# Performance work log

Measured on AMD Instinct MI355X. Metric: run time of the kernel, lower is better.

## Reference

```python
import jax, jax.numpy as jnp
from jax import lax
import numpy as np

SCORE_THRESH = 0.05
NMS_THRESH = 0.5
MAX_DET = 100
MIN_SIZE = 0.01
BBOX_CLIP = float(np.log(1000.0 / 16.0))
NEG = -1e10


def setup_inputs() -> dict:
    key = jax.random.key(0)
    ks = jax.random.split(key, 12)
    N, IN, REP, C = 2000, 256 * 7 * 7, 1024, 91
    box_features = jax.random.normal(ks[0], (N, IN), jnp.float32)
    x1 = jax.random.uniform(ks[1], (N,), jnp.float32, 0.0, 1000.0)
    y1 = jax.random.uniform(ks[2], (N,), jnp.float32, 0.0, 600.0)
    bw = jax.random.uniform(ks[3], (N,), jnp.float32, 16.0, 200.0)
    bh = jax.random.uniform(ks[4], (N,), jnp.float32, 16.0, 180.0)
    proposals = jnp.stack([x1, y1, x1 + bw, y1 + bh], axis=1)
    W1 = jax.random.normal(ks[5], (IN, REP), jnp.float32) * 0.01
    b1 = jnp.zeros((REP,), jnp.float32)
    W2 = jax.random.normal(ks[6], (REP, REP), jnp.float32) * 0.03
    b2 = jnp.zeros((REP,), jnp.float32)
    Wc = jax.random.normal(ks[7], (REP, C), jnp.float32) * 0.1
    bc = jax.random.normal(ks[8], (C,), jnp.float32) * 0.5
    Wr = jax.random.normal(ks[9], (REP, 4 * C), jnp.float32) * 0.01
    br = jnp.zeros((4 * C,), jnp.float32)
    return dict(box_features=box_features, proposals=proposals,
                W1=W1, b1=b1, W2=W2, b2=b2, Wc=Wc, bc=bc, Wr=Wr, br=br,
                image_h=800, image_w=1216)


def _nms(boxes, scores):
    """Greedy NMS with fixed trip count; scores already masked to NEG for invalid."""
    M = boxes.shape[0]
    areas = (boxes[:, 2] - boxes[:, 0]) * (boxes[:, 3] - boxes[:, 1])
    idxs = jnp.arange(M)

    def step(sm, _):
        i = jnp.argmax(sm)
        valid = sm[i] > NEG * 0.5
        b = boxes[i]
        xx1 = jnp.maximum(b[0], boxes[:, 0]); yy1 = jnp.maximum(b[1], boxes[:, 1])
        xx2 = jnp.minimum(b[2], boxes[:, 2]); yy2 = jnp.minimum(b[3], boxes[:, 3])
        inter = jnp.clip(xx2 - xx1, 0.0) * jnp.clip(yy2 - yy1, 0.0)
        iou = inter / (areas[i] + areas - inter + 1e-9)
        suppress = (iou > NMS_THRESH) | (idxs == i)
        sm = jnp.where(valid, jnp.where(suppress, NEG, sm), sm)
        return sm, jnp.where(valid, i, -1)

    _, keep = lax.scan(step, scores, None, length=MAX_DET)
    return keep  # [MAX_DET] int, -1 for padding


def reference(box_features, proposals, W1, b1, W2, b2, Wc, bc, Wr, br, image_h, image_w):
    N = box_features.shape[0]
    C = Wc.shape[1]
    # box head MLP (Linear+ReLU x2) and predictors
    h = jax.nn.relu(box_features @ W1 + b1)
    h = jax.nn.relu(h @ W2 + b2)
    class_logits = h @ Wc + bc                      # [N, C]
    box_reg = (h @ Wr + br).reshape(N, C, 4)        # [N, C, 4]
    # box decode (weights 10,10,5,5) against proposals
    pw = proposals[:, 2] - proposals[:, 0]
    ph = proposals[:, 3] - proposals[:, 1]
    pcx = proposals[:, 0] + 0.5 * pw
    pcy = proposals[:, 1] + 0.5 * ph
    dx = box_reg[..., 0] / 10.0
    dy = box_reg[..., 1] / 10.0
    dw = jnp.minimum(box_reg[..., 2] / 5.0, BBOX_CLIP)
    dh = jnp.minimum(box_reg[..., 3] / 5.0, BBOX_CLIP)
    cx = dx * pw[:, None] + pcx[:, None]
    cy = dy * ph[:, None] + pcy[:, None]
    w = jnp.exp(dw) * pw[:, None]
    hh = jnp.exp(dh) * ph[:, None]
    boxes = jnp.stack([cx - 0.5 * w, cy - 0.5 * hh, cx + 0.5 * w, cy + 0.5 * hh], axis=-1)
    scores = jax.nn.softmax(class_logits, axis=-1)
    # clip to image
    Wim = jnp.float32(image_w); Him = jnp.float32(image_h)
    boxes = jnp.stack([jnp.clip(boxes[..., 0], 0.0, Wim),
                       jnp.clip(boxes[..., 1], 0.0, Him),
                       jnp.clip(boxes[..., 2], 0.0, Wim),
                       jnp.clip(boxes[..., 3], 0.0, Him)], axis=-1)
    # drop background class, flatten to [N*(C-1)]
    boxes = boxes[:, 1:].reshape(-1, 4)
    scores = scores[:, 1:].reshape(-1)
    labels = jnp.broadcast_to(jnp.arange(1, C, dtype=jnp.int32), (N, C - 1)).reshape(-1)
    # score threshold + remove small boxes (as masking, static shapes)
    bw = boxes[:, 2] - boxes[:, 0]
    bh = boxes[:, 3] - boxes[:, 1]
    valid = (scores > SCORE_THRESH) & (bw >= MIN_SIZE) & (bh >= MIN_SIZE)
    sm = jnp.where(valid, scores, NEG)
    # class-aware (batched) NMS via per-class coordinate offsets
    off = labels.astype(boxes.dtype) * (jnp.maximum(Wim, Him) + 1.0)
    keep = _nms(boxes + off[:, None], sm)
    mask = keep >= 0
    idx = jnp.maximum(keep, 0)
    out_boxes = jnp.take(boxes, idx, axis=0) * mask[:, None]
    out_scores = jnp.take(scores, idx) * mask
    out_labels = jnp.take(labels, idx) * mask.astype(jnp.int32)
    return out_boxes, out_scores, out_labels
```

## Files before the change

### kernel.cpp

```cpp
#include <hip/hip_runtime.h>

#define CPC 2000
#define SPC 100
#define NCLS 90
#define TM 128
#define TN 128
#define TKK 16

typedef __attribute__((ext_vector_type(8))) short bf16x8;
typedef __attribute__((ext_vector_type(4))) float f32x4;
typedef __attribute__((ext_vector_type(4))) unsigned short u16x4;

__device__ __forceinline__ unsigned short f2bf_rne(float f) {
    unsigned u = __float_as_uint(f);
    return (unsigned short)((u + 0x7FFFu + ((u >> 16) & 1u)) >> 16);
}
__device__ __forceinline__ unsigned short f2bf_trunc(float f) {
    return (unsigned short)(__float_as_uint(f) >> 16);
}
__device__ __forceinline__ float bfhi_f32(float f) {
    return __uint_as_float(__float_as_uint(f) & 0xFFFF0000u);
}
__device__ __forceinline__ void async_load16(const void* g, void* l) {
    __builtin_amdgcn_global_load_lds((const __attribute__((address_space(1))) unsigned int*)g,
                                     (__attribute__((address_space(3))) unsigned int*)l, 16, 0, 0);
}
__device__ __forceinline__ int swz(int c) { return c ^ ((c >> 3) & 3); }

__device__ __forceinline__ void xcd_remap(unsigned& bx, unsigned& by, unsigned& bz)
{
    const unsigned nx = gridDim.x, ny = gridDim.y;
    const unsigned nwg = nx * ny * gridDim.z;
    unsigned lin = blockIdx.x + nx * (blockIdx.y + ny * blockIdx.z);
    if ((nwg & 7u) == 0u)
        lin = (lin & 7u) * (nwg >> 3) + (lin >> 3);
    bx = lin % nx;
    unsigned rem = lin / nx;
    by = rem % ny;
    bz = rem / ny;
}

__global__ __launch_bounds__(256) void split_transpose(
    const float* __restrict__ W, unsigned short* __restrict__ Thi,
    unsigned short* __restrict__ Tlo, int K, int N)
{
    __shared__ float tile[64][33];
    const int kt = blockIdx.x * 64, nt = blockIdx.y * 32;
    const int tx = threadIdx.x & 31, ty = threadIdx.x >> 5;
#pragma unroll
    for (int j = 0; j < 8; ++j) {
        int k = kt + ty + j * 8, n = nt + tx;
        tile[ty + j * 8][tx] = (k < K && n < N) ? W[(size_t)k * N + n] : 0.f;
    }
    __syncthreads();
#pragma unroll
    for (int j = 0; j < 4; ++j) {
        int n = nt + ty + j * 8;
        int k = kt + tx * 2;
        if (n < N && k < K) {
            float f0 = tile[tx * 2][ty + j * 8];
            float f1 = tile[tx * 2 + 1][ty + j * 8];
            unsigned hi = (unsigned)f2bf_trunc(f0) | ((unsigned)f2bf_trunc(f1) << 16);
            unsigned lo = (unsigned)f2bf_rne(f0 - bfhi_f32(f0))
                        | ((unsigned)f2bf_rne(f1 - bfhi_f32(f1)) << 16);
            *reinterpret_cast<unsigned*>(&Thi[(size_t)n * K + k]) = hi;
            *reinterpret_cast<unsigned*>(&Tlo[(size_t)n * K + k]) = lo;
        }
    }
}

__global__ __launch_bounds__(256) void split_transpose2(
    const float* __restrict__ Wa, const float* __restrict__ Wb, int Na, int Nb,
    unsigned short* __restrict__ Thi, unsigned short* __restrict__ Tlo, int K)
{
    const int N = Na + Nb;
    __shared__ float tile[64][33];
    const int kt = blockIdx.x * 64, nt = blockIdx.y * 32;
    const int tx = threadIdx.x & 31, ty = threadIdx.x >> 5;
#pragma unroll
    for (int j = 0; j < 8; ++j) {
        int k = kt + ty + j * 8, n = nt + tx;
        float v = 0.f;
        if (k < K && n < N)
            v = (n < Na) ? Wa[(size_t)k * Na + n] : Wb[(size_t)k * Nb + (n - Na)];
        tile[ty + j * 8][tx] = v;
    }
    __syncthreads();
#pragma unroll
    for (int j = 0; j < 4; ++j) {
        int n = nt + ty + j * 8;
        int k = kt + tx * 2;
        if (n < N && k < K) {
            float f0 = tile[tx * 2][ty + j * 8];
            float f1 = tile[tx * 2 + 1][ty + j * 8];
            unsigned hi = (unsigned)f2bf_trunc(f0) | ((unsigned)f2bf_trunc(f1) << 16);
            unsigned lo = (unsigned)f2bf_rne(f0 - bfhi_f32(f0))
                        | ((unsigned)f2bf_rne(f1 - bfhi_f32(f1)) << 16);
            *reinterpret_cast<unsigned*>(&Thi[(size_t)n * K + k]) = hi;
            *reinterpret_cast<unsigned*>(&Tlo[(size_t)n * K + k]) = lo;
        }
    }
}

__global__ __launch_bounds__(256, 4) void gemm_bf16x3_f32a(
    const float* __restrict__ A, const unsigned short* __restrict__ Bhi,
    const unsigned short* __restrict__ Blo, float* __restrict__ C,
    int M, int N, int K, int klen)
{
    __shared__ unsigned short Ah[2048], Al[2048], Bh[4096], Bl[4096];
    unsigned bxu, byu, bzu;
    xcd_remap(bxu, byu, bzu);
    const int tid = threadIdx.x;
    const int wv = tid >> 6, ln = tid & 63;
    const int q = ln >> 4, lm = ln & 15;
    const int m0 = byu * 64, n0 = bxu * 128;
    const int k0 = bzu * klen;
    int k1 = k0 + klen; if (k1 > K) k1 = K;
    const int bcol_t = wv * 32;

    f32x4 acc[4][2];
#pragma unroll
    for (int i = 0; i < 4; ++i)
#pragma unroll
        for (int j = 0; j < 2; ++j) acc[i][j] = (f32x4)0.f;

    int gr = m0 + (tid >> 2); if (gr >= M) gr = M - 1;
    const float* Arow = A + (size_t)gr * K + (tid & 3) * 8;
    const int apc = swz(tid);

    unsigned bsrc[2];
#pragma unroll
    for (int i = 0; i < 2; ++i) {
        int s = i * 256 + tid;
        int gn = n0 + (s >> 2); if (gn >= N) gn = N - 1;
        int qe = (s & 3) ^ ((s >> 3) & 3);
        bsrc[i] = (unsigned)gn * (unsigned)K + (unsigned)(qe * 8);
    }

    for (int kt = k0; kt < k1; kt += 32) {
#pragma unroll
        for (int i = 0; i < 2; ++i) {
            async_load16(Bhi + bsrc[i] + kt, &Bh[(i * 256 + wv * 64) * 8]);
            async_load16(Blo + bsrc[i] + kt, &Bl[(i * 256 + wv * 64) * 8]);
        }
        float4 v0 = *reinterpret_cast<const float4*>(Arow + kt);
        float4 v1 = *reinterpret_cast<const float4*>(Arow + kt + 4);
        float f[8] = {v0.x, v0.y, v0.z, v0.w, v1.x, v1.y, v1.z, v1.w};
        bf16x8 hi, lo;
#pragma unroll
        for (int e = 0; e < 8; ++e) {
            hi[e] = (short)f2bf_trunc(f[e]);
            lo[e] = (short)f2bf_rne(f[e] - bfhi_f32(f[e]));
        }
        *(bf16x8*)&Ah[apc * 8] = hi;
        *(bf16x8*)&Al[apc * 8] = lo;
        __syncthreads();

        bf16x8 afh[4], afl[4], bfh[2], bfl[2];
#pragma unroll
        for (int mi = 0; mi < 4; ++mi) {
            int p = swz((mi * 16 + lm) * 4 + q);
            afh[mi] = *(const bf16x8*)&Ah[p * 8];
            afl[mi] = *(const bf16x8*)&Al[p * 8];
        }
#pragma unroll
        for (int ni = 0; ni < 2; ++ni) {
            int p = swz((bcol_t + ni * 16 + lm) * 4 + q);
            bfh[ni] = *(const bf16x8*)&Bh[p * 8];
            bfl[ni] = *(const bf16x8*)&Bl[p * 8];
        }
#pragma unroll
        for (int mi = 0; mi < 4; ++mi)
#pragma unroll
            for (int ni = 0; ni < 2; ++ni) {
                acc[mi][ni] = __builtin_amdgcn_mfma_f32_16x16x32_bf16(afh[mi], bfh[ni], acc[mi][ni], 0, 0, 0);
                acc[mi][ni] = __builtin_amdgcn_mfma_f32_16x16x32_bf16(afl[mi], bfh[ni], acc[mi][ni], 0, 0, 0);
                acc[mi][ni] = __builtin_amdgcn_mfma_f32_16x16x32_bf16(afh[mi], bfl[ni], acc[mi][ni], 0, 0, 0);
            }
        __syncthreads();
    }

    float* Cz = C + (size_t)bzu * (size_t)M * (size_t)N;
#pragma unroll
    for (int mi = 0; mi < 4; ++mi)
#pragma unroll
        for (int ni = 0; ni < 2; ++ni)
#pragma unroll
            for (int ri = 0; ri < 4; ++ri) {
                int rr = m0 + mi * 16 + q * 4 + ri;
                int cc = n0 + bcol_t + ni * 16 + lm;
                if (rr < M && cc < N) Cz[(size_t)rr * N + cc] = acc[mi][ni][ri];
            }
}

__global__ __launch_bounds__(256, 4) void gemm_bf16x3_sa(
    const unsigned short* __restrict__ Ahi_g, const unsigned short* __restrict__ Alo_g,
    const unsigned short* __restrict__ Bhi, const unsigned short* __restrict__ Blo,
    float* __restrict__ C, int M, int N, int K, int klen)
{
    __shared__ unsigned short Ah[2048], Al[2048], Bh[4096], Bl[4096];
    unsigned bxu, byu, bzu;
    xcd_remap(bxu, byu, bzu);
    const int tid = threadIdx.x;
    const int wv = tid >> 6, ln = tid & 63;
    const int q = ln >> 4, lm = ln & 15;
    const int m0 = byu * 64, n0 = bxu * 128;
    const int k0 = bzu * klen;
    int k1 = k0 + klen; if (k1 > K) k1 = K;
    const int bcol_t = wv * 32;

    f32x4 acc[4][2];
#pragma unroll
    for (int i = 0; i < 4; ++i)
#pragma unroll
        for (int j = 0; j < 2; ++j) acc[i][j] = (f32x4)0.f;

    int agr = m0 + (tid >> 2); if (agr >= M) agr = M - 1;
    const unsigned asrc = (unsigned)agr * (unsigned)K
                        + (unsigned)(((tid & 3) ^ ((tid >> 3) & 3)) * 8);

    unsigned bsrc[2];
#pragma unroll
    for (int i = 0; i < 2; ++i) {
        int s = i * 256 + tid;
        int gn = n0 + (s >> 2); if (gn >= N) gn = N - 1;
        int qe = (s & 3) ^ ((s >> 3) & 3);
        bsrc[i] = (unsigned)gn * (unsigned)K + (unsigned)(qe * 8);
    }

    for (int kt = k0; kt < k1; kt += 32) {
        async_load16(Ahi_g + asrc + kt, &Ah[(wv * 64) * 8]);
        async_load16(Alo_g + asrc + kt, &Al[(wv * 64) * 8]);
#pragma unroll
        for (int i = 0; i < 2; ++i) {
            async_load16(Bhi + bsrc[i] + kt, &Bh[(i * 256 + wv * 64) * 8]);
            async_load16(Blo + bsrc[i] + kt, &Bl[(i * 256 + wv * 64) * 8]);
        }
        __syncthreads();

        bf16x8 afh[4], afl[4], bfh[2], bfl[2];
#pragma unroll
        for (int mi = 0; mi < 4; ++mi) {
            int p = swz((mi * 16 + lm) * 4 + q);
            afh[mi] = *(const bf16x8*)&Ah[p * 8];
            afl[mi] = *(const bf16x8*)&Al[p * 8];
        }
#pragma unroll
        for (int ni = 0; ni < 2; ++ni) {
            int p = swz((bcol_t + ni * 16 + lm) * 4 + q);
            bfh[ni] = *(const bf16x8*)&Bh[p * 8];
            bfl[ni] = *(const bf16x8*)&Bl[p * 8];
        }
#pragma unroll
        for (int mi = 0; mi < 4; ++mi)
#pragma unroll
            for (int ni = 0; ni < 2; ++ni) {
                acc[mi][ni] = __builtin_amdgcn_mfma_f32_16x16x32_bf16(afh[mi], bfh[ni], acc[mi][ni], 0, 0, 0);
                acc[mi][ni] = __builtin_amdgcn_mfma_f32_16x16x32_bf16(afl[mi], bfh[ni], acc[mi][ni], 0, 0, 0);
                acc[mi][ni] = __builtin_amdgcn_mfma_f32_16x16x32_bf16(afh[mi], bfl[ni], acc[mi][ni], 0, 0, 0);
            }
        __syncthreads();
    }

    float* Cz = C + (size_t)bzu * (size_t)M * (size_t)N;
#pragma unroll
    for (int mi = 0; mi < 4; ++mi)
#pragma unroll
        for (int ni = 0; ni < 2; ++ni)
#pragma unroll
            for (int ri = 0; ri < 4; ++ri) {
                int rr = m0 + mi * 16 + q * 4 + ri;
                int cc = n0 + bcol_t + ni * 16 + lm;
                if (rr < M && cc < N) Cz[(size_t)rr * N + cc] = acc[mi][ni][ri];
            }
}

__global__ __launch_bounds__(256) void gemm_f32(
    const float* __restrict__ A, const float* __restrict__ B,
    const float* __restrict__ bias, float* __restrict__ C,
    int M, int N, int K, int ksplit, int relu)
{
    __shared__ float As[TKK][TM + 4];
    __shared__ float Bs[TKK][TN + 4];
    const int tid = threadIdx.x;
    const int tx = tid & 15, ty = tid >> 4;
    const int m0 = blockIdx.y * TM, n0 = blockIdx.x * TN;
    const int z = blockIdx.z;
    const int kstart = z * ksplit;
    const int kend = (kstart + ksplit < K) ? (kstart + ksplit) : K;
    float* Cz = C + (size_t)z * (size_t)M * (size_t)N;
    const bool nvec = ((N & 3) == 0);

    float acc[8][8];
#pragma unroll
    for (int i = 0; i < 8; ++i)
#pragma unroll
        for (int j = 0; j < 8; ++j) acc[i][j] = 0.f;

    for (int kt = kstart; kt < kend; kt += TKK) {
#pragma unroll
        for (int l = 0; l < 2; ++l) {
            int idx = tid + l * 256;
            int rr = idx >> 2, kq = idx & 3;
            float4 v = make_float4(0.f, 0.f, 0.f, 0.f);
            int grr = m0 + rr;
            if (grr < M)
                v = *reinterpret_cast<const float4*>(A + (size_t)grr * K + kt + (kq << 2));
            As[(kq << 2) + 0][rr] = v.x;
            As[(kq << 2) + 1][rr] = v.y;
            As[(kq << 2) + 2][rr] = v.z;
            As[(kq << 2) + 3][rr] = v.w;
        }
#pragma unroll
        for (int l = 0; l < 2; ++l) {
            int idx = tid + l * 256;
            int kk = idx >> 5, nq = idx & 31;
            int gn = n0 + (nq << 2);
            const float* bp = B + (size_t)(kt + kk) * N + gn;
            float4 v;
            if (nvec && gn + 3 < N) {
                v = *reinterpret_cast<const float4*>(bp);
            } else {
                v.x = (gn + 0 < N) ? bp[0] : 0.f;
                v.y = (gn + 1 < N) ? bp[1] : 0.f;
                v.z = (gn + 2 < N) ? bp[2] : 0.f;
                v.w = (gn + 3 < N) ? bp[3] : 0.f;
            }
            *reinterpret_cast<float4*>(&Bs[kk][nq << 2]) = v;
        }
        __syncthreads();
#pragma unroll
        for (int kk = 0; kk < TKK; ++kk) {
            float a[8], b[8];
            *reinterpret_cast<float4*>(&a[0]) = *reinterpret_cast<const float4*>(&As[kk][ty * 8]);
            *reinterpret_cast<float4*>(&a[4]) = *reinterpret_cast<const float4*>(&As[kk][ty * 8 + 4]);
            *reinterpret_cast<float4*>(&b[0]) = *reinterpret_cast<const float4*>(&Bs[kk][tx * 4]);
            *reinterpret_cast<float4*>(&b[4]) = *reinterpret_cast<const float4*>(&Bs[kk][64 + tx * 4]);
#pragma unroll
            for (int i = 0; i < 8; ++i)
#pragma unroll
                for (int j = 0; j < 8; ++j)
                    acc[i][j] = fmaf(a[i], b[j], acc[i][j]);
        }
        __syncthreads();
    }
#pragma unroll
    for (int i = 0; i < 8; ++i) {
        int grr = m0 + ty * 8 + i;
        if (grr >= M) continue;
#pragma unroll
        for (int j = 0; j < 8; ++j) {
            int gc = n0 + ((j < 4) ? (tx * 4 + j) : (64 + tx * 4 + (j - 4)));
            if (gc >= N) continue;
            float v = acc[i][j];
            if (bias) v += bias[gc];
            if (relu) v = fmaxf(v, 0.f);
            Cz[(size_t)grr * N + gc] = v;
        }
    }
}

__global__ void combine_bias_act(const float* __restrict__ P, const float* __restrict__ bias,
                                 float* __restrict__ H, int total, int N, int nsplit,
                                 int pstride, int relu)
{
    int i = blockIdx.x * blockDim.x + threadIdx.x;
    if (i >= total) return;
    float s = P[i];
    for (int j = 1; j < nsplit; ++j) s += P[i + (size_t)j * (size_t)pstride];
    s += bias[i % N];
    if (relu) s = fmaxf(s, 0.f);
    H[i] = s;
}

__global__ void combine_bias_split(const float* __restrict__ P, const float* __restrict__ bias,
                                   unsigned short* __restrict__ Hhi, unsigned short* __restrict__ Hlo,
                                   int total, int N, int nsplit, int pstride, int relu)
{
    int i = (blockIdx.x * blockDim.x + threadIdx.x) * 4;
    if (i >= total) return;
    float4 s = *reinterpret_cast<const float4*>(P + i);
    for (int j = 1; j < nsplit; ++j) {
        float4 p = *reinterpret_cast<const float4*>(P + i + (size_t)j * (size_t)pstride);
        s.x += p.x; s.y += p.y; s.z += p.z; s.w += p.w;
    }
    const float4 b = *reinterpret_cast<const float4*>(bias + (i % N));
    s.x += b.x; s.y += b.y; s.z += b.z; s.w += b.w;
    if (relu) {
        s.x = fmaxf(s.x, 0.f); s.y = fmaxf(s.y, 0.f);
        s.z = fmaxf(s.z, 0.f); s.w = fmaxf(s.w, 0.f);
    }
    u16x4 hi = { f2bf_trunc(s.x), f2bf_trunc(s.y), f2bf_trunc(s.z), f2bf_trunc(s.w) };
    u16x4 lo = { f2bf_rne(s.x - bfhi_f32(s.x)), f2bf_rne(s.y - bfhi_f32(s.y)),
                 f2bf_rne(s.z - bfhi_f32(s.z)), f2bf_rne(s.w - bfhi_f32(s.w)) };
    *reinterpret_cast<u16x4*>(&Hhi[i]) = hi;
    *reinterpret_cast<u16x4*>(&Hlo[i]) = lo;
}

__global__ void combine_head(const float* __restrict__ P, const float* __restrict__ bc,
                             const float* __restrict__ br, float* __restrict__ H,
                             int total, int nsplit, int pstride)
{
    int i = (blockIdx.x * blockDim.x + threadIdx.x) * 4;
    if (i >= total) return;
    float4 s = *reinterpret_cast<const float4*>(P + i);
    for (int j = 1; j < nsplit; ++j) {
        float4 p = *reinterpret_cast<const float4*>(P + i + (size_t)j * (size_t)pstride);
        s.x += p.x; s.y += p.y; s.z += p.z; s.w += p.w;
    }
    float sv[4] = {s.x, s.y, s.z, s.w};
#pragma unroll
    for (int e = 0; e < 4; ++e) {
        int col = (i + e) % 455;
        sv[e] += (col < 91) ? bc[col] : br[col - 91];
    }
    *reinterpret_cast<float4*>(&H[i]) = make_float4(sv[0], sv[1], sv[2], sv[3]);
}

__device__ __forceinline__ float scalar_dim(const int* p)
{
    int iv = *p;
    return (iv > 0 && iv < (1 << 20)) ? (float)iv : *reinterpret_cast<const float*>(p);
}

__global__ __launch_bounds__(128) void decode_compact(
    const float* __restrict__ logits, int lstr, const float* __restrict__ breg, int bstr,
    const float4* __restrict__ proposals, const int* __restrict__ ihp,
    const int* __restrict__ iwp,
    float4* __restrict__ cbox, float* __restrict__ cscore, int* __restrict__ cn,
    int* __restrict__ ccnt)
{
    const int n = blockIdx.x;
    const int c = threadIdx.x;
    __shared__ float sl[91];
    __shared__ float red[128];
    if (c < 91) sl[c] = logits[(size_t)n * lstr + c];
    __syncthreads();
    red[c] = (c < 91) ? sl[c] : -3.0e38f;
    __syncthreads();
#pragma unroll
    for (int s = 64; s > 0; s >>= 1) {
        if (c < s) red[c] = fmaxf(red[c], red[c + s]);
        __syncthreads();
    }
    const float s_max = red[0];
    __syncthreads();
    red[c] = (c < 91) ? expf(sl[c] - s_max) : 0.f;
    __syncthreads();
#pragma unroll
    for (int s = 64; s > 0; s >>= 1) {
        if (c < s) red[c] += red[c + s];
        __syncthreads();
    }
    const float s_sum = red[0];
    if (c < 1 || c >= 91) return;

    const float score = expf(sl[c] - s_max) / s_sum;
    const float Wim = scalar_dim(iwp), Him = scalar_dim(ihp);
    float4 p = proposals[n];
    float pw = p.z - p.x, ph = p.w - p.y;
    float pcx = p.x + 0.5f * pw, pcy = p.y + 0.5f * ph;
    const float* r4 = breg + (size_t)n * bstr + c * 4;
    float dxv = r4[0] / 10.f, dyv = r4[1] / 10.f;
    const float BCLIP = 4.135166556742356f;
    float dwv = fminf(r4[2] / 5.f, BCLIP);
    float dhv = fminf(r4[3] / 5.f, BCLIP);
    float cx = dxv * pw + pcx, cy = dyv * ph + pcy;
    float w = expf(dwv) * pw, hh = expf(dhv) * ph;
    float x1 = cx - 0.5f * w, y1 = cy - 0.5f * hh;
    float x2 = cx + 0.5f * w, y2 = cy + 0.5f * hh;
    x1 = fminf(fmaxf(x1, 0.f), Wim);
    y1 = fminf(fmaxf(y1, 0.f), Him);
    x2 = fminf(fmaxf(x2, 0.f), Wim);
    y2 = fminf(fmaxf(y2, 0.f), Him);
    float bw = x2 - x1, bh = y2 - y1;
    if (score > 0.05f && bw >= 0.01f && bh >= 0.01f) {
        int cls = c - 1;
        int pos = atomicAdd(&ccnt[cls], 1);
        if (pos < CPC) {
            cbox[cls * CPC + pos] = make_float4(x1, y1, x2, y2);
            cscore[cls * CPC + pos] = score;
            cn[cls * CPC + pos] = n;
        }
    }
}

__global__ __launch_bounds__(256) void nms_class(
    const float4* __restrict__ cbox, const float* __restrict__ cscore,
    const int* __restrict__ cn, const int* __restrict__ ccnt,
    float4* __restrict__ sbox, float* __restrict__ sscore,
    unsigned long long* __restrict__ skey, int* __restrict__ scnt)
{
    const int cls = blockIdx.x;
    const int tid = threadIdx.x;
    int cnt = ccnt[cls]; if (cnt > CPC) cnt = CPC;

    __shared__ float4 cb[CPC];
    __shared__ unsigned long long keys[CPC];
    __shared__ unsigned long long red[4];
    __shared__ float4 selsh;
    __shared__ int selidx_sh;

    for (int i = tid; i < cnt; i += 256) {
        cb[i] = cbox[cls * CPC + i];
        unsigned int sb = __float_as_uint(cscore[cls * CPC + i]);
        sb ^= (sb >> 31) ? 0xFFFFFFFFu : 0x80000000u;
        unsigned int flat = (unsigned)cn[cls * CPC + i] * 90u + (unsigned)cls;
        keys[i] = ((unsigned long long)sb << 32) | (unsigned long long)(0xFFFFFFFFu - flat);
    }
    __syncthreads();

    int sel = 0;
    while (sel < SPC) {
        unsigned long long best = 0ull;
        for (int i = tid; i < cnt; i += 256) {
            unsigned long long k = keys[i];
            if (k > best) best = k;
        }
#pragma unroll
        for (int d = 32; d >= 1; d >>= 1) {
            unsigned long long o = __shfl_down(best, d, 64);
            if (o > best) best = o;
        }
        if ((tid & 63) == 0) red[tid >> 6] = best;
        __syncthreads();
        unsigned long long gbest = red[0];
        if (red[1] > gbest) gbest = red[1];
        if (red[2] > gbest) gbest = red[2];
        if (red[3] > gbest) gbest = red[3];
        if (gbest == 0ull) break;
        for (int i = tid; i < cnt; i += 256)
            if (keys[i] == gbest) { selsh = cb[i]; selidx_sh = i; }
        __syncthreads();
        float4 s = selsh;
        const int si = selidx_sh;
        const float sa = (s.z - s.x) * (s.w - s.y);
        if (tid == 0) {
            sbox[cls * SPC + sel] = s;
            unsigned int sb = (unsigned int)(gbest >> 32);
            sb ^= (sb >> 31) ? 0x80000000u : 0xFFFFFFFFu;
            sscore[cls * SPC + sel] = __uint_as_float(sb);
            skey[cls * SPC + sel] = gbest;
        }
        for (int i = tid; i < cnt; i += 256) {
            float4 b = cb[i];
            float xx1 = fmaxf(s.x, b.x), yy1 = fmaxf(s.y, b.y);
            float xx2 = fminf(s.z, b.z), yy2 = fminf(s.w, b.w);
            float inter = fmaxf(xx2 - xx1, 0.f) * fmaxf(yy2 - yy1, 0.f);
            float area = (b.z - b.x) * (b.w - b.y);
            if (3.f * inter > sa + area + 1e-9f || i == si) keys[i] = 0ull;
        }
        ++sel;
        __syncthreads();
    }
    if (tid == 0) scnt[cls] = sel;
}

__global__ __launch_bounds__(128) void nms_merge(
    const float4* __restrict__ sbox, const float* __restrict__ sscore,
    const unsigned long long* __restrict__ skey, const int* __restrict__ scnt,
    float* __restrict__ out)
{
    const int tid = threadIdx.x;
    __shared__ int head[NCLS];
    __shared__ unsigned long long red[2];
    __shared__ int selc_sh;
    if (tid < NCLS) head[tid] = 0;
    __syncthreads();

    for (int k = 0; k < 100; ++k) {
        unsigned long long key = 0ull;
        if (tid < NCLS && head[tid] < scnt[tid]) key = skey[tid * SPC + head[tid]];
        unsigned long long mykey = key;
#pragma unroll
        for (int d = 32; d >= 1; d >>= 1) {
            unsigned long long o = __shfl_down(key, d, 64);
            if (o > key) key = o;
        }
        if ((tid & 63) == 0) red[tid >> 6] = key;
        if (tid == 0) selc_sh = -1;
        __syncthreads();
        unsigned long long gbest = red[0] > red[1] ? red[0] : red[1];
        if (gbest != 0ull && mykey == gbest) selc_sh = tid;
        __syncthreads();
        const int c = selc_sh;
        if (tid == 0) {
            if (c >= 0) {
                int h = head[c];
                float4 b = sbox[c * SPC + h];
                out[k * 4 + 0] = b.x; out[k * 4 + 1] = b.y;
                out[k * 4 + 2] = b.z; out[k * 4 + 3] = b.w;
                out[400 + k] = sscore[c * SPC + h];
                out[500 + k] = (float)(c + 1);
            } else {
                out[k * 4 + 0] = 0.f; out[k * 4 + 1] = 0.f;
                out[k * 4 + 2] = 0.f; out[k * 4 + 3] = 0.f;
                out[400 + k] = 0.f; out[500 + k] = 0.f;
            }
        }
        if (c >= 0 && tid == c) head[c]++;
        __syncthreads();
    }
}

extern "C" void kernel_launch(void* const* d_in, const int* in_sizes, int n_in,
                              void* d_out, int out_size, void* d_ws, size_t ws_size,
                              hipStream_t stream)
{
    const float* bf    = (const float*)d_in[0];
    const float* props = (const float*)d_in[1];
    const float* W1    = (const float*)d_in[2];
    const float* b1    = (const float*)d_in[3];
    const float* W2    = (const float*)d_in[4];
    const float* b2    = (const float*)d_in[5];
    const float* Wc    = (const float*)d_in[6];
    const float* bc    = (const float*)d_in[7];
    const float* Wr    = (const float*)d_in[8];
    const float* br    = (const float*)d_in[9];
    const int*   ihp   = (const int*)d_in[10];
    const int*   iwp   = (const int*)d_in[11];
    float* ws  = (float*)d_ws;
    float* out = (float*)d_out;

    const size_t MN   = 2000ull * 1024ull;
    const size_t NLOG = 2000ull * 91ull;
    const size_t NREG = 2000ull * 364ull;
    const size_t NHEAD = 2000ull * 455ull;
    const size_t ws_floats = ws_size / 4;

    const size_t BT1F = 1024ull * 12544ull / 2;
    const size_t WT2F = 1024ull * 1024ull / 2;
    const size_t WHF  = 455ull * 1024ull / 2;
    const size_t NMSF = (size_t)NCLS * CPC * 6 + (size_t)NCLS * SPC * 7 + 256;
    const size_t PF   = 4 * MN;
    const size_t NEED = 2 * BT1F + 2 * WT2F + 2 * WHF + 2 * MN + NHEAD + NMSF + PF + 64;

    if (ws_floats >= NEED) {
        unsigned short* BT1hi = (unsigned short*)ws;
        unsigned short* BT1lo = (unsigned short*)(ws + BT1F);
        unsigned short* WT2hi = (unsigned short*)(ws + 2 * BT1F);
        unsigned short* WT2lo = (unsigned short*)(ws + 2 * BT1F + WT2F);
        unsigned short* WHhi  = (unsigned short*)(ws + 2 * BT1F + 2 * WT2F);
        unsigned short* WHlo  = (unsigned short*)(ws + 2 * BT1F + 2 * WT2F + WHF);
        float* H1   = ws + 2 * BT1F + 2 * WT2F + 2 * WHF;
        float* H2   = H1 + MN;
        float* HEAD = H2 + MN;
        float* CBOX   = HEAD + NHEAD;
        float* CSCORE = CBOX + (size_t)NCLS * CPC * 4;
        int*   CN     = (int*)(CSCORE + (size_t)NCLS * CPC);
        float* SBOX   = (float*)(CN + (size_t)NCLS * CPC);
        float* SSCORE = SBOX + (size_t)NCLS * SPC * 4;
        unsigned long long* SKEY = (unsigned long long*)(SSCORE + (size_t)NCLS * SPC);
        int*   CCNT = (int*)(SKEY + (size_t)NCLS * SPC);
        int*   SCNT = CCNT + NCLS;
        float* P = (float*)(SCNT + NCLS + 64);

        unsigned short* H1hi = (unsigned short*)H1;
        unsigned short* H1lo = H1hi + MN;
        unsigned short* H2hi = (unsigned short*)H2;
        unsigned short* H2lo = H2hi + MN;

        split_transpose<<<dim3(196, 32), 256, 0, stream>>>(W1, BT1hi, BT1lo, 12544, 1024);
        split_transpose<<<dim3(16, 32), 256, 0, stream>>>(W2, WT2hi, WT2lo, 1024, 1024);
        split_transpose2<<<dim3(16, 15), 256, 0, stream>>>(Wc, Wr, 91, 364, WHhi, WHlo, 1024);
        gemm_bf16x3_f32a<<<dim3(8, 32, 4), 256, 0, stream>>>(bf, BT1hi, BT1lo, P,
                                                             2000, 1024, 12544, 3136);
        combine_bias_split<<<(int)(MN / 4 / 256), 256, 0, stream>>>(P, b1, H1hi, H1lo,
                                                             (int)MN, 1024, 4, (int)MN, 1);
        gemm_bf16x3_sa<<<dim3(8, 32, 4), 256, 0, stream>>>(H1hi, H1lo, WT2hi, WT2lo, P,
                                                           2000, 1024, 1024, 256);
        combine_bias_split<<<(int)(MN / 4 / 256), 256, 0, stream>>>(P, b2, H2hi, H2lo,
                                                             (int)MN, 1024, 4, (int)MN, 1);
        gemm_bf16x3_sa<<<dim3(4, 32, 8), 256, 0, stream>>>(H2hi, H2lo, WHhi, WHlo, P,
                                                           2000, 455, 1024, 128);
        combine_head<<<(int)((NHEAD / 4 + 255) / 256), 256, 0, stream>>>(P, bc, br, HEAD,
                                                             (int)NHEAD, 8, (int)NHEAD);
        hipMemsetAsync(CCNT, 0, 2 * NCLS * sizeof(int), stream);
        decode_compact<<<2000, 128, 0, stream>>>(HEAD, 455, HEAD + 91, 455,
                                                 (const float4*)props, ihp, iwp,
                                                 (float4*)CBOX, CSCORE, CN, CCNT);
        nms_class<<<NCLS, 256, 0, stream>>>((const float4*)CBOX, CSCORE, CN, CCNT,
                                            (float4*)SBOX, SSCORE, SKEY, SCNT);
        nms_merge<<<1, 128, 0, stream>>>((const float4*)SBOX, SSCORE, SKEY, SCNT, out);
        return;
    }

    const size_t NMSF2 = (size_t)NCLS * CPC * 6 + (size_t)NCLS * SPC * 7 + 256;
    const size_t TAILF = 2 * MN + NLOG + NREG + NMSF2;
    int z1 = 2;
    if (ws_floats >= TAILF + 8 * MN) z1 = 8;
    else if (ws_floats >= TAILF + 4 * MN) z1 = 4;
    const size_t REUSE = (size_t)z1 * MN;
    int zh = (REUSE >= 8 * NREG) ? 8 : 4;

    float* P      = ws;
    float* H1     = P + REUSE;
    float* H2     = H1 + MN;
    float* LOG    = H2 + MN;
    float* BREG   = LOG + NLOG;
    float* CBOX   = BREG + NREG;
    float* CSCORE = CBOX + (size_t)NCLS * CPC * 4;
    int*   CN     = (int*)(CSCORE + (size_t)NCLS * CPC);
    float* SBOX   = (float*)(CN + (size_t)NCLS * CPC);
    float* SSCORE = SBOX + (size_t)NCLS * SPC * 4;
    unsigned long long* SKEY = (unsigned long long*)(SSCORE + (size_t)NCLS * SPC);
    int*   CCNT   = (int*)(SKEY + (size_t)NCLS * SPC);
    int*   SCNT   = CCNT + NCLS;

    gemm_f32<<<dim3(8, 16, z1), 256, 0, stream>>>(bf, W1, nullptr, P,
                                                  2000, 1024, 12544, 12544 / z1, 0);
    combine_bias_act<<<(int)((MN + 255) / 256), 256, 0, stream>>>(P, b1, H1,
                                                  (int)MN, 1024, z1, (int)MN, 1);
    gemm_f32<<<dim3(8, 16, 4), 256, 0, stream>>>(H1, W2, nullptr, P,
                                                 2000, 1024, 1024, 256, 0);
    combine_bias_act<<<(int)((MN + 255) / 256), 256, 0, stream>>>(P, b2, H2,
                                                 (int)MN, 1024, 4, (int)MN, 1);
    gemm_f32<<<dim3(1, 16, zh), 256, 0, stream>>>(H2, Wc, nullptr, P,
                                                  2000, 91, 1024, 1024 / zh, 0);
    combine_bias_act<<<(int)((NLOG + 255) / 256), 256, 0, stream>>>(P, bc, LOG,
                                                  (int)NLOG, 91, zh, (int)NLOG, 0);
    gemm_f32<<<dim3(3, 16, zh), 256, 0, stream>>>(H2, Wr, nullptr, P,
                                                  2000, 364, 1024, 1024 / zh, 0);
    combine_bias_act<<<(int)((NREG + 255) / 256), 256, 0, stream>>>(P, br, BREG,
                                                  (int)NREG, 364, zh, (int)NREG, 0);
    hipMemsetAsync(CCNT, 0, 2 * NCLS * sizeof(int), stream);
    decode_compact<<<2000, 128, 0, stream>>>(LOG, 91, BREG, 364,
                                             (const float4*)props, ihp, iwp,
                                             (float4*)CBOX, CSCORE, CN, CCNT);
    nms_class<<<NCLS, 256, 0, stream>>>((const float4*)CBOX, CSCORE, CN, CCNT,
                                        (float4*)SBOX, SSCORE, SKEY, SCNT);
    nms_merge<<<1, 128, 0, stream>>>((const float4*)SBOX, SSCORE, SKEY, SCNT, out);
}
```

Baseline: 734.7 us.

## Double-buffer B tiles and register-prefetch A in split-bf16 GEMM kernels

```diff
diff --git a/kernel.cpp b/kernel.cpp
--- a/kernel.cpp
+++ b/kernel.cpp
@@ -26,6 +26,14 @@
                                      (__attribute__((address_space(3))) unsigned int*)l, 16, 0, 0);
 }
 __device__ __forceinline__ int swz(int c) { return c ^ ((c >> 3) & 3); }
+
+__device__ __forceinline__ void split8(const float* f, bf16x8& hi, bf16x8& lo) {
+#pragma unroll
+    for (int e = 0; e < 8; ++e) {
+        hi[e] = (short)f2bf_trunc(f[e]);
+        lo[e] = (short)f2bf_rne(f[e] - bfhi_f32(f[e]));
+    }
+}
 
 __device__ __forceinline__ void xcd_remap(unsigned& bx, unsigned& by, unsigned& bz)
 {
@@ -38,6 +46,45 @@
     unsigned rem = lin / nx;
     by = rem % ny;
     bz = rem / ny;
+}
+
+__device__ __forceinline__ void stage_b(
+    const unsigned short* __restrict__ Bhi, const unsigned short* __restrict__ Blo,
+    unsigned bsrc0, unsigned bsrc1, int ks, int wv,
+    unsigned short* BhB, unsigned short* BlB)
+{
+    async_load16(Bhi + bsrc0 + ks, &BhB[(wv * 64) * 8]);
+    async_load16(Blo + bsrc0 + ks, &BlB[(wv * 64) * 8]);
+    async_load16(Bhi + bsrc1 + ks, &BhB[(256 + wv * 64) * 8]);
+    async_load16(Blo + bsrc1 + ks, &BlB[(256 + wv * 64) * 8]);
+}
+
+__device__ __forceinline__ void mfma_tile(
+    const unsigned short* __restrict__ AhB, const unsigned short* __restrict__ AlB,
+    const unsigned short* __restrict__ BhB, const unsigned short* __restrict__ BlB,
+    int lm, int q, int bcol_t, f32x4 (&acc)[4][2])
+{
+    bf16x8 afh[4], afl[4], bfh[2], bfl[2];
+#pragma unroll
+    for (int mi = 0; mi < 4; ++mi) {
+        int p = swz((mi * 16 + lm) * 4 + q);
+        afh[mi] = *(const bf16x8*)&AhB[p * 8];
+        afl[mi] = *(const bf16x8*)&AlB[p * 8];
+    }
+#pragma unroll
+    for (int ni = 0; ni < 2; ++ni) {
+        int p = swz((bcol_t + ni * 16 + lm) * 4 + q);
+        bfh[ni] = *(const bf16x8*)&BhB[p * 8];
+        bfl[ni] = *(const bf16x8*)&BlB[p * 8];
+    }
+#pragma unroll
+    for (int mi = 0; mi < 4; ++mi)
+#pragma unroll
+        for (int ni = 0; ni < 2; ++ni) {
+            acc[mi][ni] = __builtin_amdgcn_mfma_f32_16x16x32_bf16(afh[mi], bfh[ni], acc[mi][ni], 0, 0, 0);
+            acc[mi][ni] = __builtin_amdgcn_mfma_f32_16x16x32_bf16(afl[mi], bfh[ni], acc[mi][ni], 0, 0, 0);
+            acc[mi][ni] = __builtin_amdgcn_mfma_f32_16x16x32_bf16(afh[mi], bfl[ni], acc[mi][ni], 0, 0, 0);
+        }
 }
 
 __global__ __launch_bounds__(256) void split_transpose(
@@ -107,7 +154,8 @@
     const unsigned short* __restrict__ Blo, float* __restrict__ C,
     int M, int N, int K, int klen)
 {
-    __shared__ unsigned short Ah[2048], Al[2048], Bh[4096], Bl[4096];
+    __shared__ unsigned short Ah[2048], Al[2048];
+    __shared__ unsigned short Bh[2][4096], Bl[2][4096];
     unsigned bxu, byu, bzu;
     xcd_remap(bxu, byu, bzu);
     const int tid = threadIdx.x;
@@ -128,56 +176,71 @@
     const float* Arow = A + (size_t)gr * K + (tid & 3) * 8;
     const int apc = swz(tid);
 
-    unsigned bsrc[2];
-#pragma unroll
-    for (int i = 0; i < 2; ++i) {
-        int s = i * 256 + tid;
-        int gn = n0 + (s >> 2); if (gn >= N) gn = N - 1;
-        int qe = (s & 3) ^ ((s >> 3) & 3);
-        bsrc[i] = (unsigned)gn * (unsigned)K + (unsigned)(qe * 8);
-    }
-
-    for (int kt = k0; kt < k1; kt += 32) {
-#pragma unroll
-        for (int i = 0; i < 2; ++i) {
-            async_load16(Bhi + bsrc[i] + kt, &Bh[(i * 256 + wv * 64) * 8]);
-            async_load16(Blo + bsrc[i] + kt, &Bl[(i * 256 + wv * 64) * 8]);
-        }
-        float4 v0 = *reinterpret_cast<const float4*>(Arow + kt);
-        float4 v1 = *reinterpret_cast<const float4*>(Arow + kt + 4);
-        float f[8] = {v0.x, v0.y, v0.z, v0.w, v1.x, v1.y, v1.z, v1.w};
+    unsigned bsrc0, bsrc1;
+    {
+        int s0 = tid;
+        int gn0 = n0 + (s0 >> 2); if (gn0 >= N) gn0 = N - 1;
+        bsrc0 = (unsigned)gn0 * (unsigned)K + (unsigned)(((s0 & 3) ^ ((s0 >> 3) & 3)) * 8);
+        int s1 = 256 + tid;
+        int gn1 = n0 + (s1 >> 2); if (gn1 >= N) gn1 = N - 1;
+        bsrc1 = (unsigned)gn1 * (unsigned)K + (unsigned)(((s1 & 3) ^ ((s1 >> 3) & 3)) * 8);
+    }
+
+    float f[8];
+    {
+        float4 v0 = *reinterpret_cast<const float4*>(Arow + k0);
+        float4 v1 = *reinterpret_cast<const float4*>(Arow + k0 + 4);
+        f[0] = v0.x; f[1] = v0.y; f[2] = v0.z; f[3] = v0.w;
+        f[4] = v1.x; f[5] = v1.y; f[6] = v1.z; f[7] = v1.w;
+    }
+    stage_b(Bhi, Blo, bsrc0, bsrc1, k0, wv, Bh[0], Bl[0]);
+    {
         bf16x8 hi, lo;
-#pragma unroll
-        for (int e = 0; e < 8; ++e) {
-            hi[e] = (short)f2bf_trunc(f[e]);
-            lo[e] = (short)f2bf_rne(f[e] - bfhi_f32(f[e]));
-        }
+        split8(f, hi, lo);
         *(bf16x8*)&Ah[apc * 8] = hi;
         *(bf16x8*)&Al[apc * 8] = lo;
-        __syncthreads();
-
-        bf16x8 afh[4], afl[4], bfh[2], bfl[2];
-#pragma unroll
-        for (int mi = 0; mi < 4; ++mi) {
-            int p = swz((mi * 16 + lm) * 4 + q);
-            afh[mi] = *(const bf16x8*)&Ah[p * 8];
-            afl[mi] = *(const bf16x8*)&Al[p * 8];
-        }
-#pragma unroll
-        for (int ni = 0; ni < 2; ++ni) {
-            int p = swz((bcol_t + ni * 16 + lm) * 4 + q);
-            bfh[ni] = *(const bf16x8*)&Bh[p * 8];
-            bfl[ni] = *(const bf16x8*)&Bl[p * 8];
-        }
-#pragma unroll
-        for (int mi = 0; mi < 4; ++mi)
-#pragma unroll
-            for (int ni = 0; ni < 2; ++ni) {
-                acc[mi][ni] = __builtin_amdgcn_mfma_f32_16x16x32_bf16(afh[mi], bfh[ni], acc[mi][ni], 0, 0, 0);
-                acc[mi][ni] = __builtin_amdgcn_mfma_f32_16x16x32_bf16(afl[mi], bfh[ni], acc[mi][ni], 0, 0, 0);
-                acc[mi][ni] = __builtin_amdgcn_mfma_f32_16x16x32_bf16(afh[mi], bfl[ni], acc[mi][ni], 0, 0, 0);
-            }
-        __syncthreads();
+    }
+    __syncthreads();
+
+    int kt = k0;
+    for (;;) {
+        const bool n1 = kt + 32 < k1;
+        if (n1) {
+            float4 v0 = *reinterpret_cast<const float4*>(Arow + kt + 32);
+            float4 v1 = *reinterpret_cast<const float4*>(Arow + kt + 36);
+            f[0] = v0.x; f[1] = v0.y; f[2] = v0.z; f[3] = v0.w;
+            f[4] = v1.x; f[5] = v1.y; f[6] = v1.z; f[7] = v1.w;
+            stage_b(Bhi, Blo, bsrc0, bsrc1, kt + 32, wv, Bh[1], Bl[1]);
+        }
+        mfma_tile(Ah, Al, Bh[0], Bl[0], lm, q, bcol_t, acc);
+        __syncthreads();
+        if (n1) {
+            bf16x8 hi, lo;
+            split8(f, hi, lo);
+            *(bf16x8*)&Ah[apc * 8] = hi;
+            *(bf16x8*)&Al[apc * 8] = lo;
+        }
+        __syncthreads();
+        if (!n1) break;
+        const bool n2 = kt + 64 < k1;
+        if (n2) {
+            float4 v0 = *reinterpret_cast<const float4*>(Arow + kt + 64);
+            float4 v1 = *reinterpret_cast<const float4*>(Arow + kt + 68);
+            f[0] = v0.x; f[1] = v0.y; f[2] = v0.z; f[3] = v0.w;
+            f[4] = v1.x; f[5] = v1.y; f[6] = v1.z; f[7] = v1.w;
+            stage_b(Bhi, Blo, bsrc0, bsrc1, kt + 64, wv, Bh[0], Bl[0]);
+        }
+        mfma_tile(Ah, Al, Bh[1], Bl[1], lm, q, bcol_t, acc);
+        __syncthreads();
+        if (n2) {
+            bf16x8 hi, lo;
+            split8(f, hi, lo);
+            *(bf16x8*)&Ah[apc * 8] = hi;
+            *(bf16x8*)&Al[apc * 8] = lo;
+        }
+        __syncthreads();
+        if (!n2) break;
+        kt += 64;
     }
 
     float* Cz = C + (size_t)bzu * (size_t)M * (size_t)N;
@@ -198,7 +261,8 @@
     const unsigned short* __restrict__ Bhi, const unsigned short* __restrict__ Blo,
     float* __restrict__ C, int M, int N, int K, int klen)
 {
-    __shared__ unsigned short Ah[2048], Al[2048], Bh[4096], Bl[4096];
+    __shared__ unsigned short Ah[2048], Al[2048];
+    __shared__ unsigned short Bh[2][4096], Bl[2][4096];
     unsigned bxu, byu, bzu;
     xcd_remap(bxu, byu, bzu);
     const int tid = threadIdx.x;
@@ -216,50 +280,57 @@
         for (int j = 0; j < 2; ++j) acc[i][j] = (f32x4)0.f;
 
     int agr = m0 + (tid >> 2); if (agr >= M) agr = M - 1;
-    const unsigned asrc = (unsigned)agr * (unsigned)K
-                        + (unsigned)(((tid & 3) ^ ((tid >> 3) & 3)) * 8);
-
-    unsigned bsrc[2];
-#pragma unroll
-    for (int i = 0; i < 2; ++i) {
-        int s = i * 256 + tid;
-        int gn = n0 + (s >> 2); if (gn >= N) gn = N - 1;
-        int qe = (s & 3) ^ ((s >> 3) & 3);
-        bsrc[i] = (unsigned)gn * (unsigned)K + (unsigned)(qe * 8);
-    }
-
-    for (int kt = k0; kt < k1; kt += 32) {
-        async_load16(Ahi_g + asrc + kt, &Ah[(wv * 64) * 8]);
-        async_load16(Alo_g + asrc + kt, &Al[(wv * 64) * 8]);
-#pragma unroll
-        for (int i = 0; i < 2; ++i) {
-            async_load16(Bhi + bsrc[i] + kt, &Bh[(i * 256 + wv * 64) * 8]);
-            async_load16(Blo + bsrc[i] + kt, &Bl[(i * 256 + wv * 64) * 8]);
-        }
-        __syncthreads();
-
-        bf16x8 afh[4], afl[4], bfh[2], bfl[2];
-#pragma unroll
-        for (int mi = 0; mi < 4; ++mi) {
-            int p = swz((mi * 16 + lm) * 4 + q);
-            afh[mi] = *(const bf16x8*)&Ah[p * 8];
-            afl[mi] = *(const bf16x8*)&Al[p * 8];
-        }
-#pragma unroll
-        for (int ni = 0; ni < 2; ++ni) {
-            int p = swz((bcol_t + ni * 16 + lm) * 4 + q);
-            bfh[ni] = *(const bf16x8*)&Bh[p * 8];
-            bfl[ni] = *(const bf16x8*)&Bl[p * 8];
-        }
-#pragma unroll
-        for (int mi = 0; mi < 4; ++mi)
-#pragma unroll
-            for (int ni = 0; ni < 2; ++ni) {
-                acc[mi][ni] = __builtin_amdgcn_mfma_f32_16x16x32_bf16(afh[mi], bfh[ni], acc[mi][ni], 0, 0, 0);
-                acc[mi][ni] = __builtin_amdgcn_mfma_f32_16x16x32_bf16(afl[mi], bfh[ni], acc[mi][ni], 0, 0, 0);
-                acc[mi][ni] = __builtin_amdgcn_mfma_f32_16x16x32_bf16(afh[mi], bfl[ni], acc[mi][ni], 0, 0, 0);
-            }
-        __syncthreads();
+    const unsigned asrc = (unsigned)agr * (unsigned)K + (unsigned)((tid & 3) * 8);
+    const int apc = swz(tid);
+
+    unsigned bsrc0, bsrc1;
+    {
+        int s0 = tid;
+        int gn0 = n0 + (s0 >> 2); if (gn0 >= N) gn0 = N - 1;
+        bsrc0 = (unsigned)gn0 * (unsigned)K + (unsigned)(((s0 & 3) ^ ((s0 >> 3) & 3)) * 8);
+        int s1 = 256 + tid;
+        int gn1 = n0 + (s1 >> 2); if (gn1 >= N) gn1 = N - 1;
+        bsrc1 = (unsigned)gn1 * (unsigned)K + (unsigned)(((s1 & 3) ^ ((s1 >> 3) & 3)) * 8);
+    }
+
+    bf16x8 ahr = *(const bf16x8*)(Ahi_g + asrc + k0);
+    bf16x8 alr = *(const bf16x8*)(Alo_g + asrc + k0);
+    stage_b(Bhi, Blo, bsrc0, bsrc1, k0, wv, Bh[0], Bl[0]);
+    *(bf16x8*)&Ah[apc * 8] = ahr;
+    *(bf16x8*)&Al[apc * 8] = alr;
+    __syncthreads();
+
+    int kt = k0;
+    for (;;) {
+        const bool n1 = kt + 32 < k1;
+        if (n1) {
+            ahr = *(const bf16x8*)(Ahi_g + asrc + kt + 32);
+            alr = *(const bf16x8*)(Alo_g + asrc + kt + 32);
+            stage_b(Bhi, Blo, bsrc0, bsrc1, kt + 32, wv, Bh[1], Bl[1]);
+        }
+        mfma_tile(Ah, Al, Bh[0], Bl[0], lm, q, bcol_t, acc);
+        __syncthreads();
+        if (n1) {
+            *(bf16x8*)&Ah[apc * 8] = ahr;
+            *(bf16x8*)&Al[apc * 8] = alr;
+        }
+        __syncthreads();
+        if (!n1) break;
+        const bool n2 = kt + 64 < k1;
+        if (n2) {
+            ahr = *(const bf16x8*)(Ahi_g + asrc + kt + 64);
+            alr = *(const bf16x8*)(Alo_g + asrc + kt + 64);
+            stage_b(Bhi, Blo, bsrc0, bsrc1, kt + 64, wv, Bh[0], Bl[0]);
+        }
+        mfma_tile(Ah, Al, Bh[1], Bl[1], lm, q, bcol_t, acc);
+        __syncthreads();
+        if (n2) {
+            *(bf16x8*)&Ah[apc * 8] = ahr;
+            *(bf16x8*)&Al[apc * 8] = alr;
+        }
+        __syncthreads();
+        if (!n2) break;
+        kt += 64;
     }
 
     float* Cz = C + (size_t)bzu * (size_t)M * (size_t)N;
```

Result: no change. 745.6 us (+1.5%).
